# Optimization experiments

Hardware: AMD Instinct MI355X
Metric: run time of the kernel (lower is better)

The kernel has to match this reference:

```python
import jax, jax.numpy as jnp
import numpy as np

L_MAX = 119
D_MODEL = 128
N_HEADS = 4
HEAD_DIM = 32


def _rope_tables():
    # matches torch: inv_freq over arange(0,128,2)/128, t=arange(119), cast to bf16
    channel_range = jnp.arange(0, D_MODEL, 2, dtype=jnp.float32)
    inv_freq = 1.0 / (10000.0 ** (channel_range / D_MODEL))
    t = jnp.arange(L_MAX, dtype=jnp.float32)
    freqs = jnp.outer(t, inv_freq)  # (119, 64)
    return jnp.cos(freqs).astype(jnp.bfloat16), jnp.sin(freqs).astype(jnp.bfloat16)


def _apply_rotary(x, cos, sin):
    # x: (b, l, 128); half-rotation on the full model dim (pre head-split)
    l = x.shape[1]
    d = x.shape[-1] // 2
    x1, x2 = x[..., :d], x[..., d:]
    c, s = cos[:l], sin[:l]
    y1 = x1 * c + x2 * s
    y2 = x1 * (-s) + x2 * c
    return jnp.concatenate([y1, y2], axis=-1).astype(x.dtype)


def setup_inputs() -> dict:
    key = jax.random.key(0)
    k1, k2, k3, k4, k5 = jax.random.split(key, 5)
    b, l = 2048, L_MAX
    return {
        "x": jax.random.normal(k1, (b, l, D_MODEL), dtype=jnp.float32),
        "W_qkv": jax.random.normal(k2, (3 * D_MODEL, D_MODEL), dtype=jnp.float32) * 0.05,
        "b_qkv": jax.random.normal(k3, (3 * D_MODEL,), dtype=jnp.float32) * 0.02,
        "W_fc2": jax.random.normal(k4, (D_MODEL, D_MODEL), dtype=jnp.float32) * 0.05,
        "b_fc2": jax.random.normal(k5, (D_MODEL,), dtype=jnp.float32) * 0.02,
    }


def reference(x, W_qkv, b_qkv, W_fc2, b_fc2):
    b, l, _ = x.shape
    cos, sin = _rope_tables()

    qkv = x @ W_qkv.T + b_qkv  # (b, l, 384)
    q, k, v = jnp.split(qkv, 3, axis=-1)
    q = _apply_rotary(q, cos, sin)
    k = _apply_rotary(k, cos, sin)

    # faithful to source: view(b, l, 32, 4) then 'b l d h -> b h l d'
    def split_heads(t):
        return t.reshape(b, l, HEAD_DIM, N_HEADS).transpose(0, 3, 1, 2)  # (b, h, l, d)

    q, k, v = split_heads(q), split_heads(k), split_heads(v)

    scale = 1.0 / np.sqrt(HEAD_DIM)
    scores = jnp.einsum("bhld,bhmd->bhlm", q, k) * scale  # (b, h, l, l)
    causal = jnp.tril(jnp.ones((l, l), dtype=bool))
    scores = jnp.where(causal, scores, jnp.float32(-jnp.inf))
    attn = jax.nn.softmax(scores, axis=-1)
    y = jnp.einsum("bhlm,bhmd->bhld", attn, v)  # (b, h, l, d)

    # faithful to source: transpose(1,2) then view(b, l, 128) -> layout h*32+d
    y = y.transpose(0, 2, 1, 3).reshape(b, l, D_MODEL)
    y = y @ W_fc2.T + b_fc2
    return jax.nn.silu(y)
```

## Files before the change

kernel.cpp:

```cpp
#include <hip/hip_runtime.h>
#include <hip/hip_bf16.h>
#include <math.h>


#define L_SEQ 119
#define D_MODEL 128
#define SCALE 0.17677669529663687f
#define NEGINF -1e30f

typedef __bf16 bf16x8 __attribute__((ext_vector_type(8)));
typedef __bf16 bf16x2 __attribute__((ext_vector_type(2)));
typedef float f32x4 __attribute__((ext_vector_type(4)));
typedef float f32x16 __attribute__((ext_vector_type(16)));

__global__ void rope_tab_kernel(unsigned* __restrict__ tabu) {
  int i = blockIdx.x * blockDim.x + threadIdx.x;
  if (i >= L_SEQ * 64) return;
  int l = i >> 6, j = i & 63;
  float inv = 1.0f / powf(10000.0f, (float)(2 * j) / 128.0f);
  float f = (float)l * inv;
  union { bf16x2 v; unsigned u; } cs;
  cs.v[0] = (__bf16)cosf(f);
  cs.v[1] = (__bf16)sinf(f);
  tabu[i] = cs.u;
}

__global__ void wprep_kernel(const float* __restrict__ Wqkv,
                             const float* __restrict__ bqkv,
                             __bf16* __restrict__ Wb, float* __restrict__ bb2) {
  int i = blockIdx.x * 256 + threadIdx.x;
  int j = i & 7, lane = (i >> 3) & 63, ks = (i >> 9) & 7, nt = i >> 12;
  int d = lane & 31;
  int h = nt / 3, qkv = nt % 3;
  int k = ks * 16 + (lane >> 5) * 8 + j;
  Wb[i] = (__bf16)Wqkv[(qkv * 128 + d * 4 + h) * 128 + k];
  if (i < 384) {
    int nt2 = i >> 5, dd = i & 31;
    bb2[i] = bqkv[(nt2 % 3) * 128 + dd * 4 + (nt2 / 3)];
  }
}

__global__ void wprep2_kernel(const float* __restrict__ Wfc2,
                              __bf16* __restrict__ Wf2b) {
  int i = blockIdx.x * 256 + threadIdx.x;
  int j = i & 7, lane = (i >> 3) & 63, kb = (i >> 9) & 3, nt = i >> 11;
  int n = nt * 16 + (lane & 15);
  int k = kb * 32 + (lane >> 4) * 8 + j;
  Wf2b[i] = (__bf16)Wfc2[n * 128 + k];
}

__global__ __launch_bounds__(512) void fused_all(
    const float* __restrict__ x, const __bf16* __restrict__ Wb,
    const float* __restrict__ bb2, const unsigned* __restrict__ tabu,
    const __bf16* __restrict__ Wf2b, const float* __restrict__ bfc2,
    float* __restrict__ out) {
  __shared__ __align__(16) __bf16 qs[4 * 128 * 40];
  __shared__ __align__(16) __bf16 ksm[4 * 128 * 40];
  __shared__ __align__(16) __bf16 vT[4 * 32 * 128];
  __shared__ unsigned tabL[L_SEQ * 65];

  const int t = threadIdx.x, b = blockIdx.x;
  const int lane = t & 63, wv = t >> 6;
  const int ln31 = lane & 31, hi = lane >> 5;

  for (int i = t; i < L_SEQ * 64; i += 512)
    tabL[(i >> 6) * 65 + (i & 63)] = tabu[i];
  for (int i = t; i < 4 * 32 * 9; i += 512) {
    int hd = i / 9, cc = L_SEQ + i % 9, d = hd & 31;
    vT[hd * 128 + (cc ^ ((d & 7) << 3))] = (__bf16)0.0f;
  }
  __syncthreads();

  const int mt = wv & 3, g2 = wv >> 2;
  const int l_me = mt * 32 + ln31;
  const bool live = (l_me < L_SEQ);
  {
    int xr = live ? l_me : (L_SEQ - 1);
    const float* xrow = x + ((size_t)b * L_SEQ + xr) * 128;
    bf16x8 af[8];
#pragma unroll
    for (int ks = 0; ks < 8; ++ks) {
      float4 lo = *(const float4*)&xrow[ks * 16 + hi * 8];
      float4 hi4 = *(const float4*)&xrow[ks * 16 + hi * 8 + 4];
      bf16x8 v;
      v[0] = (__bf16)lo.x; v[1] = (__bf16)lo.y; v[2] = (__bf16)lo.z; v[3] = (__bf16)lo.w;
      v[4] = (__bf16)hi4.x; v[5] = (__bf16)hi4.y; v[6] = (__bf16)hi4.z; v[7] = (__bf16)hi4.w;
      af[ks] = v;
    }
#pragma unroll
    for (int r = 0; r < 3; ++r) {
      const int nt0 = g2 * 6 + 2 * r, nt1 = nt0 + 1;
      f32x16 a0 = {}, a1 = {};
#pragma unroll
      for (int ks = 0; ks < 8; ++ks) {
        bf16x8 wf0 = *(const bf16x8*)&Wb[(((nt0 * 8 + ks) * 64) + lane) * 8];
        bf16x8 wf1 = *(const bf16x8*)&Wb[(((nt1 * 8 + ks) * 64) + lane) * 8];
        a0 = __builtin_amdgcn_mfma_f32_32x32x16_bf16(wf0, af[ks], a0, 0, 0, 0);
        a1 = __builtin_amdgcn_mfma_f32_32x32x16_bf16(wf1, af[ks], a1, 0, 0, 0);
      }
#pragma unroll
      for (int e = 0; e < 2; ++e) {
        const int nt = e ? nt1 : nt0;
        const f32x16& A = e ? a1 : a0;
        const int h = nt / 3, qkv = nt % 3;
        if (qkv < 2) {
          __bf16* base = (qkv == 0) ? qs : ksm;
          if (live) {
#pragma unroll
            for (int rg = 0; rg < 8; ++rg) {
              const int c_lo = (rg & 3) + 8 * (rg >> 2);
              int d = c_lo + 4 * hi;
              union { bf16x2 v; unsigned u; } cs;
              cs.u = tabL[l_me * 65 + 4 * d + h];
              float c = (float)cs.v[0], s = (float)cs.v[1];
              float v1 = A[rg] + bb2[nt * 32 + d];
              float v2 = A[rg + 8] + bb2[nt * 32 + d + 16];
              if (qkv == 0) { v1 *= SCALE; v2 *= SCALE; }
              union { bf16x2 v; unsigned u; } pk;
              pk.v[0] = (__bf16)(v1 * c + v2 * s);
              pk.v[1] = (__bf16)(v2 * c - v1 * s);
              *(unsigned*)&base[(h * 128 + l_me) * 40 + 2 * d] = pk.u;
            }
          }
        } else {
          if (live) {
#pragma unroll
            for (int rg = 0; rg < 16; ++rg) {
              const int d = (rg & 3) + 8 * (rg >> 2) + 4 * hi;
              float val = A[rg] + bb2[nt * 32 + d];
              vT[(h * 32 + d) * 128 + (l_me ^ ((d & 7) << 3))] = (__bf16)val;
            }
          }
        }
      }
    }
  }
  __syncthreads();

  {
    const int h = wv >> 1;
#pragma unroll
    for (int ts = 0; ts < 2; ++ts) {
      const int qt = ts ? (3 - (wv & 1)) : (wv & 1);
      bf16x8 qf0 = *(const bf16x8*)&qs[(h * 128 + qt * 32 + ln31) * 40 + hi * 8];
      bf16x8 qf1 = *(const bf16x8*)&qs[(h * 128 + qt * 32 + ln31) * 40 + 16 + hi * 8];
      f32x16 s[4];
#pragma unroll
      for (int kt = 0; kt < 4; ++kt) {
        if (kt <= qt) {
          bf16x8 kf0 = *(const bf16x8*)&ksm[(h * 128 + kt * 32 + ln31) * 40 + hi * 8];
          bf16x8 kf1 = *(const bf16x8*)&ksm[(h * 128 + kt * 32 + ln31) * 40 + 16 + hi * 8];
          f32x16 z = {};
          z = __builtin_amdgcn_mfma_f32_32x32x16_bf16(kf0, qf0, z, 0, 0, 0);
          s[kt] = __builtin_amdgcn_mfma_f32_32x32x16_bf16(kf1, qf1, z, 0, 0, 0);
        }
      }
      {
#pragma unroll
        for (int rg = 0; rg < 16; ++rg) {
          const int c_lo = (rg & 3) + 8 * (rg >> 2);
#pragma unroll
          for (int kt = 0; kt < 4; ++kt) {
            if (kt == qt) {
              int crow = c_lo + 4 * hi;
              s[kt][rg] = (crow <= ln31) ? s[kt][rg] : NEGINF;
            }
          }
        }
      }
      float mx = NEGINF;
#pragma unroll
      for (int kt = 0; kt < 4; ++kt)
        if (kt <= qt)
#pragma unroll
          for (int rg = 0; rg < 16; ++rg) mx = fmaxf(mx, s[kt][rg]);
      mx = fmaxf(mx, __shfl_xor(mx, 32));
      float sum = 0.0f;
#pragma unroll
      for (int kt = 0; kt < 4; ++kt)
        if (kt <= qt)
#pragma unroll
          for (int rg = 0; rg < 16; ++rg) {
            s[kt][rg] = __expf(s[kt][rg] - mx);
            sum += s[kt][rg];
          }
      sum += __shfl_xor(sum, 32);
      float inv = 1.0f / sum;
      unsigned pk[4][8];
#pragma unroll
      for (int kt = 0; kt < 4; ++kt) {
        if (kt <= qt) {
#pragma unroll
          for (int p = 0; p < 8; ++p) {
            union { bf16x2 v; unsigned u; } w;
            w.v[0] = (__bf16)(s[kt][2 * p] * inv);
            w.v[1] = (__bf16)(s[kt][2 * p + 1] * inv);
            pk[kt][p] = w.u;
          }
        }
      }
      f32x16 o = {};
#pragma unroll
      for (int kt = 0; kt < 4; ++kt) {
        if (kt <= qt) {
#pragma unroll
          for (int m = 0; m < 2; ++m) {
            unsigned f0 = (unsigned)__shfl_xor((int)pk[kt][4 * m + 0], 32);
            unsigned f1 = (unsigned)__shfl_xor((int)pk[kt][4 * m + 1], 32);
            unsigned f2 = (unsigned)__shfl_xor((int)pk[kt][4 * m + 2], 32);
            unsigned f3 = (unsigned)__shfl_xor((int)pk[kt][4 * m + 3], 32);
            union { unsigned w[4]; bf16x8 v; } Aw;
            Aw.w[0] = hi ? f2 : pk[kt][4 * m + 0];
            Aw.w[1] = hi ? f3 : pk[kt][4 * m + 1];
            Aw.w[2] = hi ? pk[kt][4 * m + 2] : f0;
            Aw.w[3] = hi ? pk[kt][4 * m + 3] : f1;
            bf16x8 vf = *(const bf16x8*)&vT[(h * 32 + ln31) * 128 +
                ((kt * 32 + m * 16 + hi * 8) ^ ((ln31 & 7) << 3))];
            o = __builtin_amdgcn_mfma_f32_32x32x16_bf16(Aw.v, vf, o, 0, 0, 0);
          }
        }
      }
#pragma unroll
      for (int rg = 0; rg < 16; ++rg) {
        const int c_lo = (rg & 3) + 8 * (rg >> 2);
        int l = qt * 32 + c_lo + 4 * hi;
        if (l < L_SEQ)
          out[((size_t)b * L_SEQ + l) * 128 + h * 32 + ln31] = o[rg];
      }
    }
  }

  __syncthreads();
  {
    const int ln15 = lane & 15, kg = lane >> 4;
    int yr = wv * 16 + ln15;
    if (yr > L_SEQ - 1) yr = L_SEQ - 1;
    const float* yrow = out + ((size_t)b * L_SEQ + yr) * 128;
    bf16x8 af2[4];
#pragma unroll
    for (int kb = 0; kb < 4; ++kb) {
      float4 lo = *(const float4*)&yrow[kb * 32 + kg * 8];
      float4 hi4 = *(const float4*)&yrow[kb * 32 + kg * 8 + 4];
      bf16x8 v;
      v[0] = (__bf16)lo.x; v[1] = (__bf16)lo.y; v[2] = (__bf16)lo.z; v[3] = (__bf16)lo.w;
      v[4] = (__bf16)hi4.x; v[5] = (__bf16)hi4.y; v[6] = (__bf16)hi4.z; v[7] = (__bf16)hi4.w;
      af2[kb] = v;
    }
    float bc[8];
#pragma unroll
    for (int nt = 0; nt < 8; ++nt) bc[nt] = bfc2[nt * 16 + ln15];
    f32x4 acc2[8] = {};
#pragma unroll
    for (int nt = 0; nt < 8; ++nt)
#pragma unroll
      for (int kb = 0; kb < 4; ++kb)
        acc2[nt] = __builtin_amdgcn_mfma_f32_16x16x32_bf16(
            af2[kb], *(const bf16x8*)&Wf2b[(((nt * 4 + kb) * 64) + lane) * 8],
            acc2[nt], 0, 0, 0);
#pragma unroll
    for (int nt = 0; nt < 8; ++nt)
#pragma unroll
      for (int r = 0; r < 4; ++r) {
        int row = wv * 16 + kg * 4 + r, c = nt * 16 + ln15;
        if (row < L_SEQ) {
          float vv = acc2[nt][r] + bc[nt];
          out[((size_t)b * L_SEQ + row) * 128 + c] = vv / (1.0f + __expf(-vv));
        }
      }
  }
}

extern "C" void kernel_launch(void* const* d_in, const int* in_sizes, int n_in,
                              void* d_out, int out_size, void* d_ws,
                              size_t ws_size, hipStream_t stream) {
  const float* x = (const float*)d_in[0];
  const float* Wqkv = (const float*)d_in[1];
  const float* bqkv = (const float*)d_in[2];
  const float* Wfc2 = (const float*)d_in[3];
  const float* bfc2 = (const float*)d_in[4];
  float* out = (float*)d_out;

  char* ws = (char*)d_ws;
  unsigned* tabu = (unsigned*)ws;
  __bf16* Wb = (__bf16*)(ws + 30720);
  float* bb2 = (float*)(ws + 30720 + 98304);
  __bf16* Wf2b = (__bf16*)(ws + 30720 + 98304 + 1536);

  const int B = in_sizes[0] / (L_SEQ * D_MODEL);
  rope_tab_kernel<<<(L_SEQ * 64 + 255) / 256, 256, 0, stream>>>(tabu);
  wprep_kernel<<<192, 256, 0, stream>>>(Wqkv, bqkv, Wb, bb2);
  wprep2_kernel<<<64, 256, 0, stream>>>(Wfc2, Wf2b);
  fused_all<<<B, 512, 0, stream>>>(x, Wb, bb2, tabu, Wf2b, bfc2, out);
}
```

Before: 221.8 us.

## Stage weights in LDS and process heads in two passes to shrink LDS

Each block now stages the QKV weights in shared memory, half at a time, instead of reading them from global memory per wave. The projection and attention phases run in two passes of two heads each, which halves the q/k/v shared buffers and trims their row padding. The fc2 weights are also staged in the reused weight buffer, and the fc2 loop is serialized per output tile to cut register pressure. The aim is less global weight traffic and lower LDS/register use, possibly for higher occupancy, at the cost of extra barriers and reduced parallelism within each phase.

```diff
diff --git a/kernel.cpp b/kernel.cpp
--- a/kernel.cpp
+++ b/kernel.cpp
@@ -54,30 +54,23 @@
     const float* __restrict__ bb2, const unsigned* __restrict__ tabu,
     const __bf16* __restrict__ Wf2b, const float* __restrict__ bfc2,
     float* __restrict__ out) {
-  __shared__ __align__(16) __bf16 qs[4 * 128 * 40];
-  __shared__ __align__(16) __bf16 ksm[4 * 128 * 40];
-  __shared__ __align__(16) __bf16 vT[4 * 32 * 128];
+  __shared__ __align__(16) __bf16 Wlds[6 * 8 * 64 * 8];
+  __shared__ __align__(16) __bf16 qs[2 * 128 * 36];
+  __shared__ __align__(16) __bf16 ksm[2 * 128 * 36];
+  __shared__ __align__(16) __bf16 vT[2 * 32 * 128];
   __shared__ unsigned tabL[L_SEQ * 65];
 
   const int t = threadIdx.x, b = blockIdx.x;
   const int lane = t & 63, wv = t >> 6;
   const int ln31 = lane & 31, hi = lane >> 5;
-
-  for (int i = t; i < L_SEQ * 64; i += 512)
-    tabL[(i >> 6) * 65 + (i & 63)] = tabu[i];
-  for (int i = t; i < 4 * 32 * 9; i += 512) {
-    int hd = i / 9, cc = L_SEQ + i % 9, d = hd & 31;
-    vT[hd * 128 + (cc ^ ((d & 7) << 3))] = (__bf16)0.0f;
-  }
-  __syncthreads();
-
-  const int mt = wv & 3, g2 = wv >> 2;
+  const int mt = wv & 3, ng = wv >> 2;
   const int l_me = mt * 32 + ln31;
   const bool live = (l_me < L_SEQ);
+
+  bf16x8 af[8];
   {
     int xr = live ? l_me : (L_SEQ - 1);
     const float* xrow = x + ((size_t)b * L_SEQ + xr) * 128;
-    bf16x8 af[8];
 #pragma unroll
     for (int ks = 0; ks < 8; ++ks) {
       float4 lo = *(const float4*)&xrow[ks * 16 + hi * 8];
@@ -87,86 +80,101 @@
       v[4] = (__bf16)hi4.x; v[5] = (__bf16)hi4.y; v[6] = (__bf16)hi4.z; v[7] = (__bf16)hi4.w;
       af[ks] = v;
     }
-#pragma unroll
-    for (int r = 0; r < 3; ++r) {
-      const int nt0 = g2 * 6 + 2 * r, nt1 = nt0 + 1;
-      f32x16 a0 = {}, a1 = {};
+  }
+  for (int i = t; i < L_SEQ * 64; i += 512)
+    tabL[(i >> 6) * 65 + (i & 63)] = tabu[i];
+  for (int i = t; i < 2 * 32 * 9; i += 512) {
+    int hd = i / 9, cc = L_SEQ + i % 9, d = hd & 31;
+    vT[hd * 128 + (cc ^ ((d & 7) << 3))] = (__bf16)0.0f;
+  }
+  {
+    const uint4* wsrc = (const uint4*)Wb;
+    uint4 w0 = wsrc[t], w1 = wsrc[512 + t], w2 = wsrc[1024 + t];
+    uint4 w3 = wsrc[1536 + t], w4 = wsrc[2048 + t], w5 = wsrc[2560 + t];
+    uint4* wd = (uint4*)Wlds;
+    wd[t] = w0; wd[512 + t] = w1; wd[1024 + t] = w2;
+    wd[1536 + t] = w3; wd[2048 + t] = w4; wd[2560 + t] = w5;
+  }
+  __syncthreads();
+
+  for (int g = 0; g < 2; ++g) {
+#pragma unroll 1
+    for (int tt = ng * 3; tt < ng * 3 + 3; ++tt) {
+      f32x16 A = {};
 #pragma unroll
       for (int ks = 0; ks < 8; ++ks) {
-        bf16x8 wf0 = *(const bf16x8*)&Wb[(((nt0 * 8 + ks) * 64) + lane) * 8];
-        bf16x8 wf1 = *(const bf16x8*)&Wb[(((nt1 * 8 + ks) * 64) + lane) * 8];
-        a0 = __builtin_amdgcn_mfma_f32_32x32x16_bf16(wf0, af[ks], a0, 0, 0, 0);
-        a1 = __builtin_amdgcn_mfma_f32_32x32x16_bf16(wf1, af[ks], a1, 0, 0, 0);
-      }
-#pragma unroll
-      for (int e = 0; e < 2; ++e) {
-        const int nt = e ? nt1 : nt0;
-        const f32x16& A = e ? a1 : a0;
-        const int h = nt / 3, qkv = nt % 3;
-        if (qkv < 2) {
-          __bf16* base = (qkv == 0) ? qs : ksm;
-          if (live) {
-#pragma unroll
-            for (int rg = 0; rg < 8; ++rg) {
-              const int c_lo = (rg & 3) + 8 * (rg >> 2);
-              int d = c_lo + 4 * hi;
-              union { bf16x2 v; unsigned u; } cs;
-              cs.u = tabL[l_me * 65 + 4 * d + h];
-              float c = (float)cs.v[0], s = (float)cs.v[1];
-              float v1 = A[rg] + bb2[nt * 32 + d];
-              float v2 = A[rg + 8] + bb2[nt * 32 + d + 16];
-              if (qkv == 0) { v1 *= SCALE; v2 *= SCALE; }
-              union { bf16x2 v; unsigned u; } pk;
-              pk.v[0] = (__bf16)(v1 * c + v2 * s);
-              pk.v[1] = (__bf16)(v2 * c - v1 * s);
-              *(unsigned*)&base[(h * 128 + l_me) * 40 + 2 * d] = pk.u;
-            }
+        bf16x8 wf = *(const bf16x8*)&Wlds[((tt * 8 + ks) * 64 + lane) * 8];
+        A = __builtin_amdgcn_mfma_f32_32x32x16_bf16(wf, af[ks], A, 0, 0, 0);
+      }
+      const int hh2 = (tt >= 3) ? 1 : 0;
+      const int qkv = tt - 3 * hh2;
+      const int h = 2 * g + hh2;
+      const int ntg = h * 3 + qkv;
+      if (live) {
+        if (qkv == 2) {
+#pragma unroll
+          for (int rg = 0; rg < 16; ++rg) {
+            const int d = (rg & 3) + 8 * (rg >> 2) + 4 * hi;
+            float val = A[rg] + bb2[ntg * 32 + d];
+            vT[(hh2 * 32 + d) * 128 + (l_me ^ ((d & 7) << 3))] = (__bf16)val;
           }
         } else {
-          if (live) {
-#pragma unroll
-            for (int rg = 0; rg < 16; ++rg) {
-              const int d = (rg & 3) + 8 * (rg >> 2) + 4 * hi;
-              float val = A[rg] + bb2[nt * 32 + d];
-              vT[(h * 32 + d) * 128 + (l_me ^ ((d & 7) << 3))] = (__bf16)val;
-            }
-          }
-        }
-      }
-    }
-  }
-  __syncthreads();
-
-  {
-    const int h = wv >> 1;
-#pragma unroll
-    for (int ts = 0; ts < 2; ++ts) {
-      const int qt = ts ? (3 - (wv & 1)) : (wv & 1);
-      bf16x8 qf0 = *(const bf16x8*)&qs[(h * 128 + qt * 32 + ln31) * 40 + hi * 8];
-      bf16x8 qf1 = *(const bf16x8*)&qs[(h * 128 + qt * 32 + ln31) * 40 + 16 + hi * 8];
+          __bf16* base = qkv ? ksm : qs;
+#pragma unroll
+          for (int rg = 0; rg < 8; ++rg) {
+            const int c_lo = (rg & 3) + 8 * (rg >> 2);
+            int d = c_lo + 4 * hi;
+            union { bf16x2 v; unsigned u; } cs;
+            cs.u = tabL[l_me * 65 + 4 * d + h];
+            float c = (float)cs.v[0], s = (float)cs.v[1];
+            float v1 = A[rg] + bb2[ntg * 32 + d];
+            float v2 = A[rg + 8] + bb2[ntg * 32 + d + 16];
+            if (qkv == 0) { v1 *= SCALE; v2 *= SCALE; }
+            union { bf16x2 v; unsigned u; } pk;
+            pk.v[0] = (__bf16)(v1 * c + v2 * s);
+            pk.v[1] = (__bf16)(v2 * c - v1 * s);
+            *(unsigned*)&base[(hh2 * 128 + l_me) * 36 + 2 * d] = pk.u;
+          }
+        }
+      }
+    }
+    __syncthreads();
+
+    if (g == 0) {
+      const uint4* wsrc = (const uint4*)(Wb + 24576);
+      uint4 w0 = wsrc[t], w1 = wsrc[512 + t], w2 = wsrc[1024 + t];
+      uint4 w3 = wsrc[1536 + t], w4 = wsrc[2048 + t], w5 = wsrc[2560 + t];
+      uint4* wd = (uint4*)Wlds;
+      wd[t] = w0; wd[512 + t] = w1; wd[1024 + t] = w2;
+      wd[1536 + t] = w3; wd[2048 + t] = w4; wd[2560 + t] = w5;
+    } else {
+      const uint4* wsrc = (const uint4*)Wf2b;
+      uint4 w0 = wsrc[t], w1 = wsrc[512 + t], w2 = wsrc[1024 + t], w3 = wsrc[1536 + t];
+      uint4* wd = (uint4*)Wlds;
+      wd[t] = w0; wd[512 + t] = w1; wd[1024 + t] = w2; wd[1536 + t] = w3;
+    }
+
+    {
+      const int hh = wv >> 2, qt = wv & 3;
+      const int h = 2 * g + hh;
+      bf16x8 qf0 = *(const bf16x8*)&qs[(hh * 128 + qt * 32 + ln31) * 36 + hi * 8];
+      bf16x8 qf1 = *(const bf16x8*)&qs[(hh * 128 + qt * 32 + ln31) * 36 + 16 + hi * 8];
       f32x16 s[4];
 #pragma unroll
       for (int kt = 0; kt < 4; ++kt) {
         if (kt <= qt) {
-          bf16x8 kf0 = *(const bf16x8*)&ksm[(h * 128 + kt * 32 + ln31) * 40 + hi * 8];
-          bf16x8 kf1 = *(const bf16x8*)&ksm[(h * 128 + kt * 32 + ln31) * 40 + 16 + hi * 8];
+          bf16x8 kf0 = *(const bf16x8*)&ksm[(hh * 128 + kt * 32 + ln31) * 36 + hi * 8];
+          bf16x8 kf1 = *(const bf16x8*)&ksm[(hh * 128 + kt * 32 + ln31) * 36 + 16 + hi * 8];
           f32x16 z = {};
           z = __builtin_amdgcn_mfma_f32_32x32x16_bf16(kf0, qf0, z, 0, 0, 0);
           s[kt] = __builtin_amdgcn_mfma_f32_32x32x16_bf16(kf1, qf1, z, 0, 0, 0);
         }
       }
-      {
-#pragma unroll
-        for (int rg = 0; rg < 16; ++rg) {
-          const int c_lo = (rg & 3) + 8 * (rg >> 2);
-#pragma unroll
-          for (int kt = 0; kt < 4; ++kt) {
-            if (kt == qt) {
-              int crow = c_lo + 4 * hi;
-              s[kt][rg] = (crow <= ln31) ? s[kt][rg] : NEGINF;
-            }
-          }
-        }
+#pragma unroll
+      for (int rg = 0; rg < 16; ++rg) {
+        const int c_lo = (rg & 3) + 8 * (rg >> 2);
+        int crow = c_lo + 4 * hi;
+        s[qt][rg] = (crow <= ln31) ? s[qt][rg] : NEGINF;
       }
       float mx = NEGINF;
 #pragma unroll
@@ -214,7 +222,7 @@
             Aw.w[1] = hi ? f3 : pk[kt][4 * m + 1];
             Aw.w[2] = hi ? pk[kt][4 * m + 2] : f0;
             Aw.w[3] = hi ? pk[kt][4 * m + 3] : f1;
-            bf16x8 vf = *(const bf16x8*)&vT[(h * 32 + ln31) * 128 +
+            bf16x8 vf = *(const bf16x8*)&vT[(hh * 32 + ln31) * 128 +
                 ((kt * 32 + m * 16 + hi * 8) ^ ((ln31 & 7) << 3))];
             o = __builtin_amdgcn_mfma_f32_32x32x16_bf16(Aw.v, vf, o, 0, 0, 0);
           }
@@ -228,9 +236,9 @@
           out[((size_t)b * L_SEQ + l) * 128 + h * 32 + ln31] = o[rg];
       }
     }
-  }
-
-  __syncthreads();
+    __syncthreads();
+  }
+
   {
     const int ln15 = lane & 15, kg = lane >> 4;
     int yr = wv * 16 + ln15;
@@ -246,27 +254,24 @@
       v[4] = (__bf16)hi4.x; v[5] = (__bf16)hi4.y; v[6] = (__bf16)hi4.z; v[7] = (__bf16)hi4.w;
       af2[kb] = v;
     }
-    float bc[8];
-#pragma unroll
-    for (int nt = 0; nt < 8; ++nt) bc[nt] = bfc2[nt * 16 + ln15];
-    f32x4 acc2[8] = {};
-#pragma unroll
-    for (int nt = 0; nt < 8; ++nt)
+#pragma unroll 1
+    for (int nt = 0; nt < 8; ++nt) {
+      f32x4 a2 = {};
 #pragma unroll
       for (int kb = 0; kb < 4; ++kb)
-        acc2[nt] = __builtin_amdgcn_mfma_f32_16x16x32_bf16(
-            af2[kb], *(const bf16x8*)&Wf2b[(((nt * 4 + kb) * 64) + lane) * 8],
-            acc2[nt], 0, 0, 0);
-#pragma unroll
-    for (int nt = 0; nt < 8; ++nt)
+        a2 = __builtin_amdgcn_mfma_f32_16x16x32_bf16(
+            af2[kb], *(const bf16x8*)&Wlds[((nt * 4 + kb) * 64 + lane) * 8],
+            a2, 0, 0, 0);
+      float bc = bfc2[nt * 16 + ln15];
 #pragma unroll
       for (int r = 0; r < 4; ++r) {
         int row = wv * 16 + kg * 4 + r, c = nt * 16 + ln15;
         if (row < L_SEQ) {
-          float vv = acc2[nt][r] + bc[nt];
+          float vv = a2[r] + bc;
           out[((size_t)b * L_SEQ + row) * 128 + c] = vv / (1.0f + __expf(-vv));
         }
       }
+    }
   }
 }
 
```

After: 405.1 us. +82.6%, slower.

## Stage attention output in swizzled LDS instead of global round-trip; read rope table from global

Applied to the files above, without the earlier changes.

The attention output is now written as bf16 into an XOR-swizzled shared-memory tile and read back from there for the fc2 MFMA, instead of being written to the global output buffer in fp32 and reloaded. The shared rope table copy is dropped, along with its barrier, and lookups now read the global table directly. The q/k row padding shrinks from 40 to 36 elements to make room in shared memory. The causal mask loop is also simplified. The aim is to remove global memory traffic and one sync, at the cost of uncoalesced global table reads and possible LDS bank conflicts at the new stride.

```diff
diff --git a/kernel.cpp b/kernel.cpp
--- a/kernel.cpp
+++ b/kernel.cpp
@@ -54,22 +54,19 @@
     const float* __restrict__ bb2, const unsigned* __restrict__ tabu,
     const __bf16* __restrict__ Wf2b, const float* __restrict__ bfc2,
     float* __restrict__ out) {
-  __shared__ __align__(16) __bf16 qs[4 * 128 * 40];
-  __shared__ __align__(16) __bf16 ksm[4 * 128 * 40];
+  __shared__ __align__(16) __bf16 qs[4 * 128 * 36];
+  __shared__ __align__(16) __bf16 ksm[4 * 128 * 36];
   __shared__ __align__(16) __bf16 vT[4 * 32 * 128];
-  __shared__ unsigned tabL[L_SEQ * 65];
+  __shared__ __align__(16) __bf16 yL[128 * 128];
 
   const int t = threadIdx.x, b = blockIdx.x;
   const int lane = t & 63, wv = t >> 6;
   const int ln31 = lane & 31, hi = lane >> 5;
 
-  for (int i = t; i < L_SEQ * 64; i += 512)
-    tabL[(i >> 6) * 65 + (i & 63)] = tabu[i];
   for (int i = t; i < 4 * 32 * 9; i += 512) {
     int hd = i / 9, cc = L_SEQ + i % 9, d = hd & 31;
     vT[hd * 128 + (cc ^ ((d & 7) << 3))] = (__bf16)0.0f;
   }
-  __syncthreads();
 
   const int mt = wv & 3, g2 = wv >> 2;
   const int l_me = mt * 32 + ln31;
@@ -111,7 +108,7 @@
               const int c_lo = (rg & 3) + 8 * (rg >> 2);
               int d = c_lo + 4 * hi;
               union { bf16x2 v; unsigned u; } cs;
-              cs.u = tabL[l_me * 65 + 4 * d + h];
+              cs.u = tabu[l_me * 64 + 4 * d + h];
               float c = (float)cs.v[0], s = (float)cs.v[1];
               float v1 = A[rg] + bb2[nt * 32 + d];
               float v2 = A[rg + 8] + bb2[nt * 32 + d + 16];
@@ -119,7 +116,7 @@
               union { bf16x2 v; unsigned u; } pk;
               pk.v[0] = (__bf16)(v1 * c + v2 * s);
               pk.v[1] = (__bf16)(v2 * c - v1 * s);
-              *(unsigned*)&base[(h * 128 + l_me) * 40 + 2 * d] = pk.u;
+              *(unsigned*)&base[(h * 128 + l_me) * 36 + 2 * d] = pk.u;
             }
           }
         } else {
@@ -142,31 +139,24 @@
 #pragma unroll
     for (int ts = 0; ts < 2; ++ts) {
       const int qt = ts ? (3 - (wv & 1)) : (wv & 1);
-      bf16x8 qf0 = *(const bf16x8*)&qs[(h * 128 + qt * 32 + ln31) * 40 + hi * 8];
-      bf16x8 qf1 = *(const bf16x8*)&qs[(h * 128 + qt * 32 + ln31) * 40 + 16 + hi * 8];
+      bf16x8 qf0 = *(const bf16x8*)&qs[(h * 128 + qt * 32 + ln31) * 36 + hi * 8];
+      bf16x8 qf1 = *(const bf16x8*)&qs[(h * 128 + qt * 32 + ln31) * 36 + 16 + hi * 8];
       f32x16 s[4];
 #pragma unroll
       for (int kt = 0; kt < 4; ++kt) {
         if (kt <= qt) {
-          bf16x8 kf0 = *(const bf16x8*)&ksm[(h * 128 + kt * 32 + ln31) * 40 + hi * 8];
-          bf16x8 kf1 = *(const bf16x8*)&ksm[(h * 128 + kt * 32 + ln31) * 40 + 16 + hi * 8];
+          bf16x8 kf0 = *(const bf16x8*)&ksm[(h * 128 + kt * 32 + ln31) * 36 + hi * 8];
+          bf16x8 kf1 = *(const bf16x8*)&ksm[(h * 128 + kt * 32 + ln31) * 36 + 16 + hi * 8];
           f32x16 z = {};
           z = __builtin_amdgcn_mfma_f32_32x32x16_bf16(kf0, qf0, z, 0, 0, 0);
           s[kt] = __builtin_amdgcn_mfma_f32_32x32x16_bf16(kf1, qf1, z, 0, 0, 0);
         }
       }
-      {
-#pragma unroll
-        for (int rg = 0; rg < 16; ++rg) {
-          const int c_lo = (rg & 3) + 8 * (rg >> 2);
-#pragma unroll
-          for (int kt = 0; kt < 4; ++kt) {
-            if (kt == qt) {
-              int crow = c_lo + 4 * hi;
-              s[kt][rg] = (crow <= ln31) ? s[kt][rg] : NEGINF;
-            }
-          }
-        }
+#pragma unroll
+      for (int rg = 0; rg < 16; ++rg) {
+        const int c_lo = (rg & 3) + 8 * (rg >> 2);
+        int crow = c_lo + 4 * hi;
+        s[qt][rg] = (crow <= ln31) ? s[qt][rg] : NEGINF;
       }
       float mx = NEGINF;
 #pragma unroll
@@ -224,28 +214,23 @@
       for (int rg = 0; rg < 16; ++rg) {
         const int c_lo = (rg & 3) + 8 * (rg >> 2);
         int l = qt * 32 + c_lo + 4 * hi;
-        if (l < L_SEQ)
-          out[((size_t)b * L_SEQ + l) * 128 + h * 32 + ln31] = o[rg];
+        if (l < L_SEQ) {
+          int c = h * 32 + ln31;
+          yL[l * 128 + (c ^ ((l & 7) << 3))] = (__bf16)o[rg];
+        }
       }
     }
   }
-
   __syncthreads();
+
   {
     const int ln15 = lane & 15, kg = lane >> 4;
     int yr = wv * 16 + ln15;
     if (yr > L_SEQ - 1) yr = L_SEQ - 1;
-    const float* yrow = out + ((size_t)b * L_SEQ + yr) * 128;
     bf16x8 af2[4];
 #pragma unroll
-    for (int kb = 0; kb < 4; ++kb) {
-      float4 lo = *(const float4*)&yrow[kb * 32 + kg * 8];
-      float4 hi4 = *(const float4*)&yrow[kb * 32 + kg * 8 + 4];
-      bf16x8 v;
-      v[0] = (__bf16)lo.x; v[1] = (__bf16)lo.y; v[2] = (__bf16)lo.z; v[3] = (__bf16)lo.w;
-      v[4] = (__bf16)hi4.x; v[5] = (__bf16)hi4.y; v[6] = (__bf16)hi4.z; v[7] = (__bf16)hi4.w;
-      af2[kb] = v;
-    }
+    for (int kb = 0; kb < 4; ++kb)
+      af2[kb] = *(const bf16x8*)&yL[yr * 128 + ((kb * 32 + kg * 8) ^ ((yr & 7) << 3))];
     float bc[8];
 #pragma unroll
     for (int nt = 0; nt < 8; ++nt) bc[nt] = bfc2[nt * 16 + ln15];
```

Result: slower. 369.8 us (median of 2 runs) (+66.7%).

## Process heads in two passes to halve LDS and drop rope table staging

Applied to the files above, without the earlier changes.

The fused kernel now handles two heads per pass instead of all four at once. This halves the shared-memory buffers for Q, K and V, and the rope table is read straight from global memory instead of being staged in LDS. The lower LDS footprint is meant to let more blocks share a CU. In exchange, x is loaded from global twice, there is an extra barrier, and attention work per wave is split differently with a less balanced causal-tile assignment.

```diff
diff --git a/kernel.cpp b/kernel.cpp
--- a/kernel.cpp
+++ b/kernel.cpp
@@ -54,114 +54,111 @@
     const float* __restrict__ bb2, const unsigned* __restrict__ tabu,
     const __bf16* __restrict__ Wf2b, const float* __restrict__ bfc2,
     float* __restrict__ out) {
-  __shared__ __align__(16) __bf16 qs[4 * 128 * 40];
-  __shared__ __align__(16) __bf16 ksm[4 * 128 * 40];
-  __shared__ __align__(16) __bf16 vT[4 * 32 * 128];
-  __shared__ unsigned tabL[L_SEQ * 65];
+  __shared__ __align__(16) __bf16 qs[2 * 128 * 40];
+  __shared__ __align__(16) __bf16 ksm[2 * 128 * 40];
+  __shared__ __align__(16) __bf16 vT[2 * 32 * 128];
 
   const int t = threadIdx.x, b = blockIdx.x;
   const int lane = t & 63, wv = t >> 6;
   const int ln31 = lane & 31, hi = lane >> 5;
-
-  for (int i = t; i < L_SEQ * 64; i += 512)
-    tabL[(i >> 6) * 65 + (i & 63)] = tabu[i];
-  for (int i = t; i < 4 * 32 * 9; i += 512) {
+  const int mt = wv & 3, hg = wv >> 2;
+  const int l_me = mt * 32 + ln31;
+  const bool live = (l_me < L_SEQ);
+
+  for (int i = t; i < 2 * 32 * 9; i += 512) {
     int hd = i / 9, cc = L_SEQ + i % 9, d = hd & 31;
     vT[hd * 128 + (cc ^ ((d & 7) << 3))] = (__bf16)0.0f;
   }
-  __syncthreads();
-
-  const int mt = wv & 3, g2 = wv >> 2;
-  const int l_me = mt * 32 + ln31;
-  const bool live = (l_me < L_SEQ);
-  {
-    int xr = live ? l_me : (L_SEQ - 1);
-    const float* xrow = x + ((size_t)b * L_SEQ + xr) * 128;
-    bf16x8 af[8];
-#pragma unroll
-    for (int ks = 0; ks < 8; ++ks) {
-      float4 lo = *(const float4*)&xrow[ks * 16 + hi * 8];
-      float4 hi4 = *(const float4*)&xrow[ks * 16 + hi * 8 + 4];
-      bf16x8 v;
-      v[0] = (__bf16)lo.x; v[1] = (__bf16)lo.y; v[2] = (__bf16)lo.z; v[3] = (__bf16)lo.w;
-      v[4] = (__bf16)hi4.x; v[5] = (__bf16)hi4.y; v[6] = (__bf16)hi4.z; v[7] = (__bf16)hi4.w;
-      af[ks] = v;
-    }
-#pragma unroll
-    for (int r = 0; r < 3; ++r) {
-      const int nt0 = g2 * 6 + 2 * r, nt1 = nt0 + 1;
-      f32x16 a0 = {}, a1 = {};
+
+#pragma unroll
+  for (int g = 0; g < 2; ++g) {
+    if (g) __syncthreads();
+
+    {
+      int xr = live ? l_me : (L_SEQ - 1);
+      const float* xrow = x + ((size_t)b * L_SEQ + xr) * 128;
+      bf16x8 af[8];
 #pragma unroll
       for (int ks = 0; ks < 8; ++ks) {
-        bf16x8 wf0 = *(const bf16x8*)&Wb[(((nt0 * 8 + ks) * 64) + lane) * 8];
-        bf16x8 wf1 = *(const bf16x8*)&Wb[(((nt1 * 8 + ks) * 64) + lane) * 8];
-        a0 = __builtin_amdgcn_mfma_f32_32x32x16_bf16(wf0, af[ks], a0, 0, 0, 0);
-        a1 = __builtin_amdgcn_mfma_f32_32x32x16_bf16(wf1, af[ks], a1, 0, 0, 0);
-      }
-#pragma unroll
-      for (int e = 0; e < 2; ++e) {
-        const int nt = e ? nt1 : nt0;
-        const f32x16& A = e ? a1 : a0;
-        const int h = nt / 3, qkv = nt % 3;
-        if (qkv < 2) {
-          __bf16* base = (qkv == 0) ? qs : ksm;
+        float4 lo = *(const float4*)&xrow[ks * 16 + hi * 8];
+        float4 hi4 = *(const float4*)&xrow[ks * 16 + hi * 8 + 4];
+        bf16x8 v;
+        v[0] = (__bf16)lo.x; v[1] = (__bf16)lo.y; v[2] = (__bf16)lo.z; v[3] = (__bf16)lo.w;
+        v[4] = (__bf16)hi4.x; v[5] = (__bf16)hi4.y; v[6] = (__bf16)hi4.z; v[7] = (__bf16)hi4.w;
+        af[ks] = v;
+      }
+      const int h = 2 * g + hg;
+      const int ntq = h * 3;
+      {
+        f32x16 a0 = {}, a1 = {};
+#pragma unroll
+        for (int ks = 0; ks < 8; ++ks) {
+          bf16x8 wf0 = *(const bf16x8*)&Wb[(((ntq * 8 + ks) * 64) + lane) * 8];
+          bf16x8 wf1 = *(const bf16x8*)&Wb[((((ntq + 1) * 8 + ks) * 64) + lane) * 8];
+          a0 = __builtin_amdgcn_mfma_f32_32x32x16_bf16(wf0, af[ks], a0, 0, 0, 0);
+          a1 = __builtin_amdgcn_mfma_f32_32x32x16_bf16(wf1, af[ks], a1, 0, 0, 0);
+        }
+#pragma unroll
+        for (int e = 0; e < 2; ++e) {
+          const f32x16& A = e ? a1 : a0;
+          const int nt = ntq + e;
+          __bf16* base = e ? ksm : qs;
           if (live) {
 #pragma unroll
             for (int rg = 0; rg < 8; ++rg) {
               const int c_lo = (rg & 3) + 8 * (rg >> 2);
               int d = c_lo + 4 * hi;
               union { bf16x2 v; unsigned u; } cs;
-              cs.u = tabL[l_me * 65 + 4 * d + h];
+              cs.u = tabu[l_me * 64 + 4 * d + h];
               float c = (float)cs.v[0], s = (float)cs.v[1];
               float v1 = A[rg] + bb2[nt * 32 + d];
               float v2 = A[rg + 8] + bb2[nt * 32 + d + 16];
-              if (qkv == 0) { v1 *= SCALE; v2 *= SCALE; }
+              if (e == 0) { v1 *= SCALE; v2 *= SCALE; }
               union { bf16x2 v; unsigned u; } pk;
               pk.v[0] = (__bf16)(v1 * c + v2 * s);
               pk.v[1] = (__bf16)(v2 * c - v1 * s);
-              *(unsigned*)&base[(h * 128 + l_me) * 40 + 2 * d] = pk.u;
+              *(unsigned*)&base[(hg * 128 + l_me) * 40 + 2 * d] = pk.u;
             }
           }
-        } else {
-          if (live) {
-#pragma unroll
-            for (int rg = 0; rg < 16; ++rg) {
-              const int d = (rg & 3) + 8 * (rg >> 2) + 4 * hi;
-              float val = A[rg] + bb2[nt * 32 + d];
-              vT[(h * 32 + d) * 128 + (l_me ^ ((d & 7) << 3))] = (__bf16)val;
-            }
+        }
+      }
+      {
+        f32x16 a2 = {};
+#pragma unroll
+        for (int ks = 0; ks < 8; ++ks) {
+          bf16x8 wf2 = *(const bf16x8*)&Wb[((((ntq + 2) * 8 + ks) * 64) + lane) * 8];
+          a2 = __builtin_amdgcn_mfma_f32_32x32x16_bf16(wf2, af[ks], a2, 0, 0, 0);
+        }
+        if (live) {
+#pragma unroll
+          for (int rg = 0; rg < 16; ++rg) {
+            const int d = (rg & 3) + 8 * (rg >> 2) + 4 * hi;
+            float val = a2[rg] + bb2[(ntq + 2) * 32 + d];
+            vT[(hg * 32 + d) * 128 + (l_me ^ ((d & 7) << 3))] = (__bf16)val;
           }
         }
       }
     }
-  }
-  __syncthreads();
-
-  {
-    const int h = wv >> 1;
-#pragma unroll
-    for (int ts = 0; ts < 2; ++ts) {
-      const int qt = ts ? (3 - (wv & 1)) : (wv & 1);
-      bf16x8 qf0 = *(const bf16x8*)&qs[(h * 128 + qt * 32 + ln31) * 40 + hi * 8];
-      bf16x8 qf1 = *(const bf16x8*)&qs[(h * 128 + qt * 32 + ln31) * 40 + 16 + hi * 8];
+    __syncthreads();
+
+    {
+      const int lh = wv & 1, qt = wv >> 1;
+      const int h = 2 * g + lh;
+      bf16x8 qf0 = *(const bf16x8*)&qs[(lh * 128 + qt * 32 + ln31) * 40 + hi * 8];
+      bf16x8 qf1 = *(const bf16x8*)&qs[(lh * 128 + qt * 32 + ln31) * 40 + 16 + hi * 8];
       f32x16 s[4];
 #pragma unroll
       for (int kt = 0; kt < 4; ++kt) {
         if (kt <= qt) {
-          bf16x8 kf0 = *(const bf16x8*)&ksm[(h * 128 + kt * 32 + ln31) * 40 + hi * 8];
-          bf16x8 kf1 = *(const bf16x8*)&ksm[(h * 128 + kt * 32 + ln31) * 40 + 16 + hi * 8];
+          bf16x8 kf0 = *(const bf16x8*)&ksm[(lh * 128 + kt * 32 + ln31) * 40 + hi * 8];
+          bf16x8 kf1 = *(const bf16x8*)&ksm[(lh * 128 + kt * 32 + ln31) * 40 + 16 + hi * 8];
           f32x16 z = {};
           z = __builtin_amdgcn_mfma_f32_32x32x16_bf16(kf0, qf0, z, 0, 0, 0);
           s[kt] = __builtin_amdgcn_mfma_f32_32x32x16_bf16(kf1, qf1, z, 0, 0, 0);
-        }
-      }
-      {
-#pragma unroll
-        for (int rg = 0; rg < 16; ++rg) {
-          const int c_lo = (rg & 3) + 8 * (rg >> 2);
-#pragma unroll
-          for (int kt = 0; kt < 4; ++kt) {
-            if (kt == qt) {
+          if (kt == qt) {
+#pragma unroll
+            for (int rg = 0; rg < 16; ++rg) {
+              const int c_lo = (rg & 3) + 8 * (rg >> 2);
               int crow = c_lo + 4 * hi;
               s[kt][rg] = (crow <= ln31) ? s[kt][rg] : NEGINF;
             }
@@ -214,7 +211,7 @@
             Aw.w[1] = hi ? f3 : pk[kt][4 * m + 1];
             Aw.w[2] = hi ? pk[kt][4 * m + 2] : f0;
             Aw.w[3] = hi ? pk[kt][4 * m + 3] : f1;
-            bf16x8 vf = *(const bf16x8*)&vT[(h * 32 + ln31) * 128 +
+            bf16x8 vf = *(const bf16x8*)&vT[(lh * 32 + ln31) * 128 +
                 ((kt * 32 + m * 16 + hi * 8) ^ ((ln31 & 7) << 3))];
             o = __builtin_amdgcn_mfma_f32_32x32x16_bf16(Aw.v, vf, o, 0, 0, 0);
           }
@@ -229,8 +226,8 @@
       }
     }
   }
-
   __syncthreads();
+
   {
     const int ln15 = lane & 15, kg = lane >> 4;
     int yr = wv * 16 + ln15;
```

Result: slower. 274.8 us (+23.9%).
